# Performance work log

Hardware: AMD Instinct MI355X
Metric: run time of the kernel (lower is better)

Reference implementation:

```python
import jax, jax.numpy as jnp
import numpy as np

NUM_EMBEDDINGS = 512
EMBEDDING_DIM = 64
COMMITMENT_COST = 0.25
DECAY = 0.99
EPSILON = 1e-05


def setup_inputs() -> dict:
    key = jax.random.key(0)
    k1, k2, k3 = jax.random.split(key, 3)
    inputs = jax.random.normal(k1, (32, 64, 64, EMBEDDING_DIM), dtype=jnp.float32)
    emb_w = jax.random.normal(k2, (NUM_EMBEDDINGS, EMBEDDING_DIM), dtype=jnp.float32)
    ema_cluster_size = jnp.ones((NUM_EMBEDDINGS,), dtype=jnp.float32)
    ema_w = jax.random.normal(k3, (NUM_EMBEDDINGS, EMBEDDING_DIM), dtype=jnp.float32)
    return {"inputs": inputs, "emb_w": emb_w,
            "ema_cluster_size": ema_cluster_size, "ema_w": ema_w}


def reference(inputs, emb_w, ema_cluster_size, ema_w):
    """VQ-VAE EMA quantizer forward (training=True path).

    inputs:           [B, H, W, D]  NHWC latents
    emb_w:            [K, D]        codebook (pre-update)
    ema_cluster_size: [K]           EMA cluster-size buffer
    ema_w:            [K, D]        EMA weight buffer
    """
    B, H, W, D = inputs.shape
    K = emb_w.shape[0]
    flat = inputs.reshape(-1, D)                                  # [N, D]

    distances = (jnp.sum(flat * flat, axis=1, keepdims=True)
                 - 2.0 * flat @ emb_w.T
                 + jnp.sum(emb_w * emb_w, axis=1))
    encoding_indices = jnp.argmin(distances, axis=1)              # [N]
    encodings = jax.nn.one_hot(encoding_indices, K, dtype=flat.dtype)  # [N, K]

    # --- EMA codebook update (buffer math; no gradient flows here) ---
    counts = jax.lax.stop_gradient(jnp.sum(encodings, axis=0))    # [K]
    cs = ema_cluster_size * DECAY + (1.0 - DECAY) * counts
    n = jnp.sum(cs)
    cs = (cs + EPSILON) / (n + K * EPSILON) * n                   # Laplace smoothing
    dw = jax.ops.segment_sum(jax.lax.stop_gradient(flat),
                             encoding_indices, num_segments=K)    # [K, D]
    new_ema_w = ema_w * DECAY + (1.0 - DECAY) * dw
    new_emb = new_ema_w / cs[:, None]                             # updated codebook

    # Quantize with the updated codebook (gather)
    quantized = new_emb[encoding_indices].reshape(B, H, W, D)

    # Commitment loss (quantized is detached)
    e_latent_loss = jnp.mean((jax.lax.stop_gradient(quantized) - inputs) ** 2)
    loss = COMMITMENT_COST * e_latent_loss

    # Straight-through estimator
    quantized_st = inputs + jax.lax.stop_gradient(quantized - inputs)

    avg_probs = jnp.mean(encodings, axis=0)
    perplexity = jnp.exp(-jnp.sum(avg_probs * jnp.log(avg_probs + 1e-10)))

    # NHWC -> NCHW as in the original return
    return loss, jnp.transpose(quantized_st, (0, 3, 1, 2)), perplexity, encodings
```

## Files before the change

### kernel.cpp

```cpp
#include <hip/hip_runtime.h>

#define DIM 64
#define K_CODES 512
#define N_VEC 131072
#define CREP 16
#define DREP 64
#define Q_OFF 1
#define PERP_OFF 8388609
#define ENC_OFF 8388610

#define NF4_TOTAL 16777215
#define ENC_A_F4  9437184
#define ENC_A_BLOCKS 768
#define ENC_B_BLOCKS 768
#define DW_BLOCKS 512
#define QZ_BLOCKS 2048

using bfrag = __attribute__((ext_vector_type(8))) short;
using ffrag = __attribute__((ext_vector_type(4))) float;

__device__ __forceinline__ void split3(float x, short& h0, short& h1, short& h2)
{
    unsigned u0 = __float_as_uint(x);
    h0 = (short)(u0 >> 16);
    float r = x - __uint_as_float(u0 & 0xFFFF0000u);
    unsigned u1 = __float_as_uint(r);
    h1 = (short)(u1 >> 16);
    float r2 = r - __uint_as_float(u1 & 0xFFFF0000u);
    h2 = (short)(__float_as_uint(r2) >> 16);
}

__global__ __launch_bounds__(256) void epack_ee_kernel(
    const float* __restrict__ emb_w,
    bfrag* __restrict__ epack,
    float* __restrict__ ee,
    float* __restrict__ crep,
    float* __restrict__ lossac)
{
    __shared__ float part[2][16][8];
    const int tl = threadIdx.x;
    const int t = blockIdx.x * 256 + tl;
    const int lane = t & 63;
    const int db = (t >> 6) & 1;
    const int ctl = tl >> 7;
    const int ct = t >> 7;
    const int r16 = lane & 15, quad = lane >> 4;
    const int c  = ct * 16 + r16;
    const int d0 = db * 32 + quad * 8;
    const float* src = emb_w + (size_t)c * DIM + d0;

    crep[t] = 0.f;
    crep[4096 + t] = 0.f;
    if (t == 0) lossac[0] = 0.f;

    bfrag f0, f1, f2;
    float ssum = 0.f;
#pragma unroll
    for (int j = 0; j < 8; ++j) {
        const float x = src[j];
        ssum = fmaf(x, x, ssum);
        short a, b, cc;
        split3(x, a, b, cc);
        f0[j] = a; f1[j] = b; f2[j] = cc;
    }
    const int base = (ct * 2 + db) * 3;
    epack[(base + 0) * 64 + lane] = f0;
    epack[(base + 1) * 64 + lane] = f1;
    epack[(base + 2) * 64 + lane] = f2;

    part[ctl][r16][db * 4 + quad] = ssum;
    __syncthreads();
    if (tl < 32) {
        const int cl = tl >> 4, r = tl & 15;
        float s = 0.f;
#pragma unroll
        for (int i = 0; i < 8; ++i) s += part[cl][r][i];
        ee[(blockIdx.x * 2 + cl) * 16 + r] = s;
    }
}

__global__ __launch_bounds__(256, 2) void argmin_mfma_kernel(
    const float* __restrict__ inputs,
    const bfrag* __restrict__ epack,
    const float* __restrict__ eeg,
    int* __restrict__ idx,
    float* __restrict__ counts_rep,
    float* __restrict__ dwrep)
{
    const int t = threadIdx.x;
    const int lane = t & 63;
    const int r16 = lane & 15;
    const int quad = lane >> 4;
    const size_t v0 = (size_t)blockIdx.x * 256 + (t >> 6) * 64;

    {
        float4* z4 = reinterpret_cast<float4*>(dwrep) + (size_t)blockIdx.x * 1024;
        const float4 z = make_float4(0.f, 0.f, 0.f, 0.f);
#pragma unroll
        for (int i = 0; i < 4; ++i) z4[i * 256 + t] = z;
    }

    bfrag xf[4][2][3];
#pragma unroll
    for (int rt = 0; rt < 4; ++rt)
#pragma unroll
        for (int db = 0; db < 2; ++db) {
            const float* src = inputs + (v0 + rt * 16 + r16) * DIM + db * 32 + quad * 8;
            const float4 va = *reinterpret_cast<const float4*>(src);
            const float4 vb = *reinterpret_cast<const float4*>(src + 4);
            float vals[8] = {va.x, va.y, va.z, va.w, vb.x, vb.y, vb.z, vb.w};
            bfrag f0, f1, f2;
#pragma unroll
            for (int j = 0; j < 8; ++j) {
                short a, b, c;
                split3(vals[j], a, b, c);
                f0[j] = a; f1[j] = b; f2[j] = c;
            }
            xf[rt][db][0] = f0; xf[rt][db][1] = f1; xf[rt][db][2] = f2;
        }

    float best[4][4];
    int bestk[4][4];
#pragma unroll
    for (int a = 0; a < 4; ++a)
#pragma unroll
        for (int b = 0; b < 4; ++b) { best[a][b] = 3.4e38f; bestk[a][b] = 0; }

    constexpr int PI[6] = {0, 0, 1, 0, 2, 1};
    constexpr int PJ[6] = {0, 1, 0, 2, 0, 1};

#pragma unroll 2
    for (int ct = 0; ct < 32; ++ct) {
        bfrag e[2][3];
#pragma unroll
        for (int db = 0; db < 2; ++db)
#pragma unroll
            for (int s = 0; s < 3; ++s)
                e[db][s] = epack[((ct * 2 + db) * 3 + s) * 64 + lane];
        const float eel = eeg[ct * 16 + r16];

        ffrag acc[4];
#pragma unroll
        for (int rt = 0; rt < 4; ++rt) acc[rt] = (ffrag){0.f, 0.f, 0.f, 0.f};

#pragma unroll
        for (int db = 0; db < 2; ++db)
#pragma unroll
            for (int p = 0; p < 6; ++p)
#pragma unroll
                for (int rt = 0; rt < 4; ++rt)
                    acc[rt] = __builtin_amdgcn_mfma_f32_16x16x32_bf16(
                        xf[rt][db][PI[p]], e[db][PJ[p]], acc[rt], 0, 0, 0);

        const int kc = ct * 16 + r16;
#pragma unroll
        for (int rt = 0; rt < 4; ++rt)
#pragma unroll
            for (int rg = 0; rg < 4; ++rg) {
                const float dist = fmaf(-2.f, acc[rt][rg], eel);
                if (dist < best[rt][rg]) { best[rt][rg] = dist; bestk[rt][rg] = kc; }
            }
    }

#pragma unroll
    for (int rt = 0; rt < 4; ++rt)
#pragma unroll
        for (int rg = 0; rg < 4; ++rg) {
            float b = best[rt][rg];
            int k = bestk[rt][rg];
#pragma unroll
            for (int m = 1; m < 16; m <<= 1) {
                const float ob = __shfl_xor(b, m, 64);
                const int ok = __shfl_xor(k, m, 64);
                if (ob < b || (ob == b && ok < k)) { b = ob; k = ok; }
            }
            bestk[rt][rg] = k;
        }

    if (r16 == 0) {
        float* crep = counts_rep + (blockIdx.x & (CREP - 1)) * K_CODES;
#pragma unroll
        for (int rt = 0; rt < 4; ++rt)
#pragma unroll
            for (int rg = 0; rg < 4; ++rg) {
                const int v = rt * 16 + quad * 4 + rg;
                const int k = bestk[rt][rg];
                idx[v0 + v] = k;
                atomicAdd(&crep[k], 1.0f);
            }
    }
}

__device__ __forceinline__ void enc_body_write(
    const int* __restrict__ idx, float* __restrict__ enc,
    int eb, int nblocks, size_t g_lo, size_t g_hi, int t)
{
    float4* body = reinterpret_cast<float4*>(enc + 2);
    const size_t stride = (size_t)nblocks * 256;
    for (size_t g = g_lo + (size_t)eb * 256 + t; g < g_hi; g += stride) {
        const size_t e0 = 4 * g + 2;
        const int r0 = (int)(e0 >> 9);
        const int r1 = (int)((e0 + 3) >> 9);
        const int i0 = idx[r0];
        const int i1 = (r1 != r0) ? idx[r1] : i0;
        float4 v;
        v.x = ((int)(e0 & 511) == i0) ? 1.f : 0.f;
        v.y = ((int)((e0 + 1) & 511) == (((e0 + 1) >> 9) == (size_t)r0 ? i0 : i1)) ? 1.f : 0.f;
        v.z = ((int)((e0 + 2) & 511) == (((e0 + 2) >> 9) == (size_t)r0 ? i0 : i1)) ? 1.f : 0.f;
        v.w = ((int)((e0 + 3) & 511) == (((e0 + 3) >> 9) == (size_t)r0 ? i0 : i1)) ? 1.f : 0.f;
        body[g] = v;
    }
}

__global__ __launch_bounds__(256) void mix1_kernel(
    const float* __restrict__ inputs,
    const int* __restrict__ idx,
    float* __restrict__ enc,
    float* __restrict__ dwrep)
{
    const int g = blockIdx.x / 5, r = blockIdx.x % 5;
    const int t = threadIdx.x;

    if (r < 2) {
        __shared__ int sIdx[256];
        const int bid = g * 2 + r;
        const size_t vbase = (size_t)bid * 256;
        sIdx[t] = idx[vbase + t];
        __syncthreads();
        const int w = t >> 6, lane = t & 63;
        const int v0 = w * 64;
#pragma unroll 4
        for (int j = 0; j < 64; ++j) {
            const int v = v0 + j;
            const int k = sIdx[v];
            const float xv = inputs[(vbase + v) * DIM + lane];
            atomicAdd(&dwrep[((size_t)(v & (DREP - 1)) << 15) + (k << 6) + lane], xv);
        }
    } else {
        const int eb = g * 3 + (r - 2);
        enc_body_write(idx, enc, eb, ENC_A_BLOCKS, 0, ENC_A_F4, t);
        if (eb == 0 && t == 0) {
            const int k0 = idx[0];
            enc[0] = (k0 == 0) ? 1.f : 0.f;
            enc[1] = (k0 == 1) ? 1.f : 0.f;
        }
    }
}

__global__ __launch_bounds__(256) void emaBF_kernel(
    const float* __restrict__ counts_rep,
    const float* __restrict__ ema_cs,
    const float* __restrict__ dwrep,
    const float* __restrict__ ema_w,
    float* __restrict__ new_emb,
    float* __restrict__ perp_out)
{
    __shared__ float scs[K_CODES];
    __shared__ float red[256];
    const int t = threadIdx.x;

    float c0 = 0.f, c1 = 0.f;
#pragma unroll
    for (int r = 0; r < CREP; ++r) {
        c0 += counts_rep[r * K_CODES + 2 * t];
        c1 += counts_rep[r * K_CODES + 2 * t + 1];
    }
    const float cs0 = ema_cs[2 * t] * 0.99f + 0.01f * c0;
    const float cs1 = ema_cs[2 * t + 1] * 0.99f + 0.01f * c1;

    red[t] = cs0 + cs1;
    __syncthreads();
    for (int s = 128; s > 0; s >>= 1) {
        if (t < s) red[t] += red[t + s];
        __syncthreads();
    }
    const float n = red[0];
    __syncthreads();

    const float scale = n / (n + (float)K_CODES * 1e-5f);
    scs[2 * t]     = (cs0 + 1e-5f) * scale;
    scs[2 * t + 1] = (cs1 + 1e-5f) * scale;

    if (blockIdx.x == 0) {
        const float p0 = c0 * (1.0f / (float)N_VEC);
        const float p1 = c1 * (1.0f / (float)N_VEC);
        red[t] = p0 * logf(p0 + 1e-10f) + p1 * logf(p1 + 1e-10f);
        __syncthreads();
        for (int s = 128; s > 0; s >>= 1) {
            if (t < s) red[t] += red[t + s];
            __syncthreads();
        }
        if (t == 0) perp_out[0] = expf(-red[0]);
    }
    __syncthreads();

    const int k = blockIdx.x * 4 + (t >> 6);
    const int e = k * DIM + (t & 63);
    float dwv = 0.f;
#pragma unroll
    for (int r = 0; r < DREP; ++r) dwv += dwrep[((size_t)r << 15) + e];
    const float v = ema_w[e] * 0.99f + 0.01f * dwv;
    new_emb[e] = v / scs[k];
}

__global__ __launch_bounds__(256) void mix2_kernel(
    const float* __restrict__ inputs,
    const int* __restrict__ idx,
    const float* __restrict__ new_emb,
    float* __restrict__ out_q,
    float* __restrict__ loss_accum,
    float* __restrict__ enc)
{
    const int g = blockIdx.x / 11, r = blockIdx.x % 11;
    const int t = threadIdx.x;

    if (r < 8) {
        __shared__ int sIdx[64];
        __shared__ float tile[DIM][65];
        __shared__ float wsum[4];

        const int bh = g * 8 + r;
        const int b = bh >> 6, h = bh & 63;

        if (t < 64) sIdx[t] = idx[bh * 64 + t];
        __syncthreads();

        const float* inRow = inputs + (size_t)bh * 64 * DIM;
        const int d = t & 63;
        const int wg = t >> 6;
        float lsum = 0.f;
#pragma unroll
        for (int p = 0; p < 16; ++p) {
            const int w = wg * 16 + p;
            const float xv = inRow[w * DIM + d];
            const float qv = new_emb[sIdx[w] * DIM + d];
            const float diff = qv - xv;
            tile[d][w] = xv + diff;
            lsum = fmaf(diff, diff, lsum);
        }
        __syncthreads();

        const int w2 = t & 63;
        const int dg = t >> 6;
#pragma unroll
        for (int p = 0; p < 16; ++p) {
            const int d2 = dg * 16 + p;
            out_q[(((size_t)b * DIM + d2) * 64 + h) * 64 + w2] = tile[d2][w2];
        }

        for (int off = 32; off > 0; off >>= 1) lsum += __shfl_down(lsum, off);
        if ((t & 63) == 0) wsum[t >> 6] = lsum;
        __syncthreads();
        if (t == 0) atomicAdd(loss_accum, (wsum[0] + wsum[1]) + (wsum[2] + wsum[3]));
    } else {
        const int eb = g * 3 + (r - 8);
        enc_body_write(idx, enc, eb, ENC_B_BLOCKS, ENC_A_F4, NF4_TOTAL, t);
        if (eb == 0 && t == 0) {
            const int kL = idx[N_VEC - 1];
            enc[67108862] = (kL == 510) ? 1.f : 0.f;
            enc[67108863] = (kL == 511) ? 1.f : 0.f;
        }
    }
}

__global__ void finalize_kernel(const float* __restrict__ loss_accum,
                                float* __restrict__ out_loss)
{
    out_loss[0] = 0.25f * (loss_accum[0] / 8388608.0f);
}

extern "C" void kernel_launch(void* const* d_in, const int* in_sizes, int n_in,
                              void* d_out, int out_size, void* d_ws, size_t ws_size,
                              hipStream_t stream)
{
    const float* inputs = (const float*)d_in[0];
    const float* emb_w  = (const float*)d_in[1];
    const float* ema_cs = (const float*)d_in[2];
    const float* ema_w  = (const float*)d_in[3];
    float* out = (float*)d_out;
    float* ws  = (float*)d_ws;

    int*   idxbuf  = (int*)ws;
    float* crep    = ws + 131072;
    float* lossac  = ws + 139264;
    float* csbuf   = ws + 139265;
    float* eebuf   = ws + 139777;
    float* nemb    = ws + 140289;
    bfrag* epack   = (bfrag*)(ws + 173060);
    (void)csbuf;

    float* dwrep = out + 16;

    epack_ee_kernel<<<16, 256, 0, stream>>>(emb_w, epack, eebuf, crep, lossac);

    argmin_mfma_kernel<<<N_VEC / 256, 256, 0, stream>>>(
        inputs, epack, eebuf, idxbuf, crep, dwrep);

    mix1_kernel<<<DW_BLOCKS + ENC_A_BLOCKS, 256, 0, stream>>>(
        inputs, idxbuf, out + ENC_OFF, dwrep);

    emaBF_kernel<<<K_CODES / 4, 256, 0, stream>>>(
        crep, ema_cs, dwrep, ema_w, nemb, out + PERP_OFF);

    mix2_kernel<<<QZ_BLOCKS + ENC_B_BLOCKS, 256, 0, stream>>>(
        inputs, idxbuf, nemb, out + Q_OFF, lossac, out + ENC_OFF);

    finalize_kernel<<<1, 1, 0, stream>>>(lossac, out);
}
```

Baseline: 185.8 us.

## Zero-fill one-hot encodings alongside argmin, then scatter ones in dw kernel

The 256 MB one-hot encoding output is no longer computed from the indices. Extra blocks in the argmin kernel zero-fill it concurrently with the MFMA distance work. The dw-accumulation kernel then scatters a single 1.0 per vector, and the quantize kernel no longer carries encoding-writer blocks. This removes the index lookups and compares from the bulk encoding write and overlaps that write with compute-bound argmin. The risk is that fill blocks compete with argmin blocks for CUs and that the ordering between zero-fill and scatter now depends on kernel boundaries.

```diff
diff --git a/kernel.cpp b/kernel.cpp
--- a/kernel.cpp
+++ b/kernel.cpp
@@ -10,9 +10,7 @@
 #define ENC_OFF 8388610
 
 #define NF4_TOTAL 16777215
-#define ENC_A_F4  9437184
-#define ENC_A_BLOCKS 768
-#define ENC_B_BLOCKS 768
+#define FILL_BLOCKS 1024
 #define DW_BLOCKS 512
 #define QZ_BLOCKS 2048
 
@@ -79,22 +77,40 @@
     }
 }
 
-__global__ __launch_bounds__(256, 2) void argmin_mfma_kernel(
+__global__ __launch_bounds__(256, 2) void mixA_kernel(
     const float* __restrict__ inputs,
     const bfrag* __restrict__ epack,
     const float* __restrict__ eeg,
     int* __restrict__ idx,
     float* __restrict__ counts_rep,
-    float* __restrict__ dwrep)
-{
+    float* __restrict__ dwrep,
+    float* __restrict__ enc)
+{
+    const int role = blockIdx.x % 3;
+    const int g = blockIdx.x / 3;
     const int t = threadIdx.x;
+
+    if (role != 0) {
+        const int fb = g * 2 + (role - 1);
+        float4* body = reinterpret_cast<float4*>(enc + 2);
+        const size_t stride = (size_t)FILL_BLOCKS * 256;
+        const float4 z = make_float4(0.f, 0.f, 0.f, 0.f);
+        for (size_t i = (size_t)fb * 256 + t; i < NF4_TOTAL; i += stride)
+            body[i] = z;
+        if (fb == 0 && t == 0) {
+            enc[0] = 0.f; enc[1] = 0.f;
+            enc[67108862] = 0.f; enc[67108863] = 0.f;
+        }
+        return;
+    }
+
     const int lane = t & 63;
     const int r16 = lane & 15;
     const int quad = lane >> 4;
-    const size_t v0 = (size_t)blockIdx.x * 256 + (t >> 6) * 64;
+    const size_t v0 = (size_t)g * 256 + (t >> 6) * 64;
 
     {
-        float4* z4 = reinterpret_cast<float4*>(dwrep) + (size_t)blockIdx.x * 1024;
+        float4* z4 = reinterpret_cast<float4*>(dwrep) + (size_t)g * 1024;
         const float4 z = make_float4(0.f, 0.f, 0.f, 0.f);
 #pragma unroll
         for (int i = 0; i < 4; ++i) z4[i * 256 + t] = z;
@@ -178,7 +194,7 @@
         }
 
     if (r16 == 0) {
-        float* crep = counts_rep + (blockIdx.x & (CREP - 1)) * K_CODES;
+        float* crep = counts_rep + (g & (CREP - 1)) * K_CODES;
 #pragma unroll
         for (int rt = 0; rt < 4; ++rt)
 #pragma unroll
@@ -191,59 +207,28 @@
     }
 }
 
-__device__ __forceinline__ void enc_body_write(
-    const int* __restrict__ idx, float* __restrict__ enc,
-    int eb, int nblocks, size_t g_lo, size_t g_hi, int t)
-{
-    float4* body = reinterpret_cast<float4*>(enc + 2);
-    const size_t stride = (size_t)nblocks * 256;
-    for (size_t g = g_lo + (size_t)eb * 256 + t; g < g_hi; g += stride) {
-        const size_t e0 = 4 * g + 2;
-        const int r0 = (int)(e0 >> 9);
-        const int r1 = (int)((e0 + 3) >> 9);
-        const int i0 = idx[r0];
-        const int i1 = (r1 != r0) ? idx[r1] : i0;
-        float4 v;
-        v.x = ((int)(e0 & 511) == i0) ? 1.f : 0.f;
-        v.y = ((int)((e0 + 1) & 511) == (((e0 + 1) >> 9) == (size_t)r0 ? i0 : i1)) ? 1.f : 0.f;
-        v.z = ((int)((e0 + 2) & 511) == (((e0 + 2) >> 9) == (size_t)r0 ? i0 : i1)) ? 1.f : 0.f;
-        v.w = ((int)((e0 + 3) & 511) == (((e0 + 3) >> 9) == (size_t)r0 ? i0 : i1)) ? 1.f : 0.f;
-        body[g] = v;
-    }
-}
-
 __global__ __launch_bounds__(256) void mix1_kernel(
     const float* __restrict__ inputs,
     const int* __restrict__ idx,
     float* __restrict__ enc,
     float* __restrict__ dwrep)
 {
-    const int g = blockIdx.x / 5, r = blockIdx.x % 5;
+    __shared__ int sIdx[256];
     const int t = threadIdx.x;
-
-    if (r < 2) {
-        __shared__ int sIdx[256];
-        const int bid = g * 2 + r;
-        const size_t vbase = (size_t)bid * 256;
-        sIdx[t] = idx[vbase + t];
-        __syncthreads();
-        const int w = t >> 6, lane = t & 63;
-        const int v0 = w * 64;
+    const size_t vbase = (size_t)blockIdx.x * 256;
+    sIdx[t] = idx[vbase + t];
+    __syncthreads();
+
+    enc[(vbase + t) * (size_t)K_CODES + sIdx[t]] = 1.0f;
+
+    const int w = t >> 6, lane = t & 63;
+    const int v0 = w * 64;
 #pragma unroll 4
-        for (int j = 0; j < 64; ++j) {
-            const int v = v0 + j;
-            const int k = sIdx[v];
-            const float xv = inputs[(vbase + v) * DIM + lane];
-            atomicAdd(&dwrep[((size_t)(v & (DREP - 1)) << 15) + (k << 6) + lane], xv);
-        }
-    } else {
-        const int eb = g * 3 + (r - 2);
-        enc_body_write(idx, enc, eb, ENC_A_BLOCKS, 0, ENC_A_F4, t);
-        if (eb == 0 && t == 0) {
-            const int k0 = idx[0];
-            enc[0] = (k0 == 0) ? 1.f : 0.f;
-            enc[1] = (k0 == 1) ? 1.f : 0.f;
-        }
+    for (int j = 0; j < 64; ++j) {
+        const int v = v0 + j;
+        const int k = sIdx[v];
+        const float xv = inputs[(vbase + v) * DIM + lane];
+        atomicAdd(&dwrep[((size_t)(v & (DREP - 1)) << 15) + (k << 6) + lane], xv);
     }
 }
 
@@ -303,64 +288,51 @@
     new_emb[e] = v / scs[k];
 }
 
-__global__ __launch_bounds__(256) void mix2_kernel(
+__global__ __launch_bounds__(256) void quantize_kernel(
     const float* __restrict__ inputs,
     const int* __restrict__ idx,
     const float* __restrict__ new_emb,
     float* __restrict__ out_q,
-    float* __restrict__ loss_accum,
-    float* __restrict__ enc)
-{
-    const int g = blockIdx.x / 11, r = blockIdx.x % 11;
+    float* __restrict__ loss_accum)
+{
+    __shared__ int sIdx[64];
+    __shared__ float tile[DIM][65];
+    __shared__ float wsum[4];
+
+    const int bh = blockIdx.x;
+    const int b = bh >> 6, h = bh & 63;
     const int t = threadIdx.x;
 
-    if (r < 8) {
-        __shared__ int sIdx[64];
-        __shared__ float tile[DIM][65];
-        __shared__ float wsum[4];
-
-        const int bh = g * 8 + r;
-        const int b = bh >> 6, h = bh & 63;
-
-        if (t < 64) sIdx[t] = idx[bh * 64 + t];
-        __syncthreads();
-
-        const float* inRow = inputs + (size_t)bh * 64 * DIM;
-        const int d = t & 63;
-        const int wg = t >> 6;
-        float lsum = 0.f;
-#pragma unroll
-        for (int p = 0; p < 16; ++p) {
-            const int w = wg * 16 + p;
-            const float xv = inRow[w * DIM + d];
-            const float qv = new_emb[sIdx[w] * DIM + d];
-            const float diff = qv - xv;
-            tile[d][w] = xv + diff;
-            lsum = fmaf(diff, diff, lsum);
-        }
-        __syncthreads();
-
-        const int w2 = t & 63;
-        const int dg = t >> 6;
-#pragma unroll
-        for (int p = 0; p < 16; ++p) {
-            const int d2 = dg * 16 + p;
-            out_q[(((size_t)b * DIM + d2) * 64 + h) * 64 + w2] = tile[d2][w2];
-        }
-
-        for (int off = 32; off > 0; off >>= 1) lsum += __shfl_down(lsum, off);
-        if ((t & 63) == 0) wsum[t >> 6] = lsum;
-        __syncthreads();
-        if (t == 0) atomicAdd(loss_accum, (wsum[0] + wsum[1]) + (wsum[2] + wsum[3]));
-    } else {
-        const int eb = g * 3 + (r - 8);
-        enc_body_write(idx, enc, eb, ENC_B_BLOCKS, ENC_A_F4, NF4_TOTAL, t);
-        if (eb == 0 && t == 0) {
-            const int kL = idx[N_VEC - 1];
-            enc[67108862] = (kL == 510) ? 1.f : 0.f;
-            enc[67108863] = (kL == 511) ? 1.f : 0.f;
-        }
-    }
+    if (t < 64) sIdx[t] = idx[bh * 64 + t];
+    __syncthreads();
+
+    const float* inRow = inputs + (size_t)bh * 64 * DIM;
+    const int d = t & 63;
+    const int wg = t >> 6;
+    float lsum = 0.f;
+#pragma unroll
+    for (int p = 0; p < 16; ++p) {
+        const int w = wg * 16 + p;
+        const float xv = inRow[w * DIM + d];
+        const float qv = new_emb[sIdx[w] * DIM + d];
+        const float diff = qv - xv;
+        tile[d][w] = xv + diff;
+        lsum = fmaf(diff, diff, lsum);
+    }
+    __syncthreads();
+
+    const int w2 = t & 63;
+    const int dg = t >> 6;
+#pragma unroll
+    for (int p = 0; p < 16; ++p) {
+        const int d2 = dg * 16 + p;
+        out_q[(((size_t)b * DIM + d2) * 64 + h) * 64 + w2] = tile[d2][w2];
+    }
+
+    for (int off = 32; off > 0; off >>= 1) lsum += __shfl_down(lsum, off);
+    if ((t & 63) == 0) wsum[t >> 6] = lsum;
+    __syncthreads();
+    if (t == 0) atomicAdd(loss_accum, (wsum[0] + wsum[1]) + (wsum[2] + wsum[3]));
 }
 
 __global__ void finalize_kernel(const float* __restrict__ loss_accum,
@@ -383,27 +355,25 @@
     int*   idxbuf  = (int*)ws;
     float* crep    = ws + 131072;
     float* lossac  = ws + 139264;
-    float* csbuf   = ws + 139265;
     float* eebuf   = ws + 139777;
     float* nemb    = ws + 140289;
     bfrag* epack   = (bfrag*)(ws + 173060);
-    (void)csbuf;
 
     float* dwrep = out + 16;
 
     epack_ee_kernel<<<16, 256, 0, stream>>>(emb_w, epack, eebuf, crep, lossac);
 
-    argmin_mfma_kernel<<<N_VEC / 256, 256, 0, stream>>>(
-        inputs, epack, eebuf, idxbuf, crep, dwrep);
-
-    mix1_kernel<<<DW_BLOCKS + ENC_A_BLOCKS, 256, 0, stream>>>(
+    mixA_kernel<<<3 * 512, 256, 0, stream>>>(
+        inputs, epack, eebuf, idxbuf, crep, dwrep, out + ENC_OFF);
+
+    mix1_kernel<<<DW_BLOCKS, 256, 0, stream>>>(
         inputs, idxbuf, out + ENC_OFF, dwrep);
 
     emaBF_kernel<<<K_CODES / 4, 256, 0, stream>>>(
         crep, ema_cs, dwrep, ema_w, nemb, out + PERP_OFF);
 
-    mix2_kernel<<<QZ_BLOCKS + ENC_B_BLOCKS, 256, 0, stream>>>(
-        inputs, idxbuf, nemb, out + Q_OFF, lossac, out + ENC_OFF);
+    quantize_kernel<<<QZ_BLOCKS, 256, 0, stream>>>(
+        inputs, idxbuf, nemb, out + Q_OFF, lossac);
 
     finalize_kernel<<<1, 1, 0, stream>>>(lossac, out);
 }
```

After: 207.0 us. 11.4% more time.
